# Kernel tuning notes

Measured on AMD Instinct MI355X. Metric: run time of the kernel, lower is better.

## Reference

```python
import jax, jax.numpy as jnp
import numpy as np

T = 256          # tokens
H = 1024         # hidden_size
E = 64           # num_experts
I = 512          # routed intermediate_size
SI = 2048        # shared_expert_intermediate_size
TOP_K = 6
N_GROUP = 8
TOPK_GROUP = 4
ROUTED_SCALE = 2.5


def setup_inputs() -> dict:
    key = jax.random.key(0)
    ks = jax.random.split(key, 9)
    s = 0.02
    return {
        "hidden_states": jax.random.normal(ks[0], (T, H), jnp.float32),
        "gate_w": jax.random.normal(ks[1], (E, H), jnp.float32) * s,
        "e_bias": jax.random.normal(ks[2], (E,), jnp.float32) * 0.01,
        "w1": jax.random.normal(ks[3], (E, I, H), jnp.float32) * s,  # gate proj
        "w3": jax.random.normal(ks[4], (E, I, H), jnp.float32) * s,  # up proj
        "w2": jax.random.normal(ks[5], (E, H, I), jnp.float32) * s,  # down proj
        "ws_gate": jax.random.normal(ks[6], (SI, H), jnp.float32) * s,
        "ws_up": jax.random.normal(ks[7], (SI, H), jnp.float32) * s,
        "ws_down": jax.random.normal(ks[8], (H, SI), jnp.float32) * s,
    }


def _noaux_tc_routing(logits, e_bias):
    # DeepSeek-V3 group-limited sigmoid routing (is_thop=False path).
    scores = jax.nn.sigmoid(logits)                         # [T, E]
    swb = scores + e_bias                                   # bias only picks experts
    t, e = scores.shape
    g = swb.reshape(t, N_GROUP, e // N_GROUP)
    group_scores = jax.lax.top_k(g, 2)[0].sum(-1)           # top-2 sum per group [T, G]
    _, gidx = jax.lax.top_k(group_scores, TOPK_GROUP)
    gmask = jax.nn.one_hot(gidx, N_GROUP, dtype=scores.dtype).sum(-2)  # [T, G]
    smask = jnp.repeat(gmask, e // N_GROUP, axis=-1)        # [T, E]
    _, tidx = jax.lax.top_k(swb * smask, TOP_K)
    nmask = jax.nn.one_hot(tidx, e, dtype=scores.dtype).sum(-2)
    s = scores * nmask
    s = s / (s.sum(-1, keepdims=True) + 1e-20) * ROUTED_SCALE  # [T, E], TOP_K nonzeros
    # torch code returns topk(values, indices) of s; s itself is the dense
    # combine-weight matrix with exactly those values scattered at the indices.
    return s


def reference(hidden_states, gate_w, e_bias, w1, w3, w2, ws_gate, ws_up, ws_down):
    x = hidden_states
    # gate: cublas_mm with fp32 output
    logits = (x @ gate_w.T).astype(jnp.float32)             # [T, E]
    cw = _noaux_tc_routing(logits, e_bias)                  # [T, E] combine weights

    # routed experts: gated MLP per expert, combined by routing weights
    h1 = jnp.einsum('th,eih->tei', x, w1)
    h3 = jnp.einsum('th,eih->tei', x, w3)
    act = jax.nn.silu(h1) * h3                              # [T, E, I]
    eo = jnp.einsum('tei,ehi->teh', act, w2)                # [T, E, H]
    routed = jnp.einsum('teh,te->th', eo, cw.astype(x.dtype))

    # shared experts: GatedMLP
    shared = (jax.nn.silu(x @ ws_gate.T) * (x @ ws_up.T)) @ ws_down.T

    return shared + routed
```

## Files before the change

### kernel.cpp

```cpp
#include <hip/hip_runtime.h>
#include <math.h>

#define T_TOK 256
#define H_DIM 1024
#define E_NUM 64
#define I_DIM 512
#define SI_DIM 2048

#define BN 64
#define BM 32
#define BK 64
#define LDB 72

typedef __attribute__((ext_vector_type(8))) short short8;
typedef __attribute__((ext_vector_type(8))) __bf16 bf16x8;
typedef __attribute__((ext_vector_type(4))) float floatx4;
typedef __attribute__((ext_vector_type(4))) unsigned short ushort4v;

static __device__ __forceinline__ unsigned short f2bf(float f) {
  unsigned u = __float_as_uint(f);
  u += 0x7FFFu + ((u >> 16) & 1u);
  return (unsigned short)(u >> 16);
}

static __device__ __forceinline__ ushort4v pack4(floatx4 v) {
  ushort4v b;
  b[0] = f2bf(v[0]); b[1] = f2bf(v[1]); b[2] = f2bf(v[2]); b[3] = f2bf(v[3]);
  return b;
}

static __device__ __forceinline__ floatx4 mfma16(bf16x8 a, bf16x8 b, floatx4 c) {
  return __builtin_amdgcn_mfma_f32_16x16x32_bf16(a, b, c, 0, 0, 0);
}

__global__ __launch_bounds__(256) void gate_route_kernel(
    const float* __restrict__ x, const float* __restrict__ gw,
    const float* __restrict__ ebias, unsigned short* __restrict__ xbf,
    int* __restrict__ cnt, int* __restrict__ tok_list,
    float* __restrict__ wt_list) {
  const int t = blockIdx.x;
  const int j = threadIdx.x;
  __shared__ float xs[H_DIM];
  __shared__ double pd[4 * 64];

  floatx4 v = ((const floatx4*)(x + (size_t)t * H_DIM))[j];
  xs[4 * j + 0] = v[0]; xs[4 * j + 1] = v[1];
  xs[4 * j + 2] = v[2]; xs[4 * j + 3] = v[3];
  ((ushort4v*)(xbf + (size_t)t * H_DIM))[j] = pack4(v);
  __syncthreads();

  const int e = j & 63, ch = j >> 6;
  const float* wr = gw + (size_t)e * H_DIM + ch * 256;
  const float* xc = xs + ch * 256;
  double acc = 0.0;
  for (int i = 0; i < 64; ++i) {
    floatx4 w = ((const floatx4*)wr)[i];
    acc += (double)xc[4 * i + 0] * (double)w[0]
         + (double)xc[4 * i + 1] * (double)w[1]
         + (double)xc[4 * i + 2] * (double)w[2]
         + (double)xc[4 * i + 3] * (double)w[3];
  }
  pd[ch * 64 + e] = acc;
  __syncthreads();

  if (j < 64) {
    const int lane = j;
    const double logit = pd[lane] + pd[64 + lane] + pd[128 + lane] + pd[192 + lane];
    const double score = 1.0 / (1.0 + exp(-logit));
    const double swb = score + (double)ebias[lane];

    double m1 = swb, m2 = -1.0e300;
    #pragma unroll
    for (int d = 1; d < 8; d <<= 1) {
      double o1 = __shfl_xor(m1, d);
      double o2 = __shfl_xor(m2, d);
      double hi = fmax(m1, o1), lo = fmin(m1, o1);
      m1 = hi;
      m2 = fmax(lo, fmax(m2, o2));
    }
    const double gscore = m1 + m2;

    double gs[8];
    #pragma unroll
    for (int g = 0; g < 8; ++g) gs[g] = __shfl(gscore, g << 3);
    unsigned gsel = 0;
    #pragma unroll
    for (int it = 0; it < 4; ++it) {
      int best = 0; double bv = -1.0e300;
      #pragma unroll
      for (int g = 0; g < 8; ++g) {
        bool taken = (gsel >> g) & 1u;
        if (!taken && gs[g] > bv) { bv = gs[g]; best = g; }
      }
      gsel |= 1u << best;
    }

    double key = ((gsel >> (lane >> 3)) & 1u) ? swb : -1.0e300;
    int selected = 0;
    for (int it = 0; it < 6; ++it) {
      double vv = key; int idx = lane;
      #pragma unroll
      for (int d = 1; d < 64; d <<= 1) {
        double ov = __shfl_xor(vv, d);
        int oi = __shfl_xor(idx, d);
        if (ov > vv || (ov == vv && oi < idx)) { vv = ov; idx = oi; }
      }
      if (lane == idx) { selected = 1; key = -1.0e300; }
    }

    double ssum = selected ? score : 0.0;
    #pragma unroll
    for (int d = 1; d < 64; d <<= 1) ssum += __shfl_xor(ssum, d);

    if (selected) {
      float wgt = (float)(score / (ssum + 1e-20) * 2.5);
      int p = atomicAdd(&cnt[lane], 1);
      tok_list[lane * T_TOK + p] = t;
      wt_list[lane * T_TOK + p] = wgt;
    }
  }
}

__global__ __launch_bounds__(256) void routed_gu_kernel(
    const unsigned short* __restrict__ xbf, const float* __restrict__ w1,
    const float* __restrict__ w3, const int* __restrict__ cnt,
    const int* __restrict__ tok_list, unsigned short* __restrict__ act_r) {
  __shared__ unsigned short sBg[BN * LDB];
  __shared__ unsigned short sBu[BN * LDB];
  __shared__ unsigned short sA[BM * LDB];
  __shared__ int stok[BM];

  const int e = blockIdx.x >> 3;
  const int n0 = (blockIdx.x & 7) * BN;
  const int j = threadIdx.x;
  const int wv = j >> 6, lane = j & 63;
  const int q = lane >> 4, c = lane & 15;
  const int ne = cnt[e];
  const int* tl = tok_list + e * T_TOK;
  unsigned short* ap = act_r + (size_t)e * T_TOK * I_DIM;
  const float* wgB = w1 + ((size_t)e * I_DIM + n0) * H_DIM;
  const float* wuB = w3 + ((size_t)e * I_DIM + n0) * H_DIM;

  const int wrow = j >> 4;
  const int wcol = (j & 15) * 4;
  const int arow = j >> 3;
  const int acol = (j & 7) * 8;

  for (int m0 = 0; m0 < ne; m0 += BM) {
    __syncthreads();
    if (j < BM) {
      int r = m0 + j;
      stok[j] = (r < ne) ? tl[r] : 0;
    }
    floatx4 ag0 = (floatx4)0.0f, ag1 = (floatx4)0.0f;
    floatx4 au0 = (floatx4)0.0f, au1 = (floatx4)0.0f;
    for (int k0 = 0; k0 < H_DIM; k0 += BK) {
      __syncthreads();
      #pragma unroll
      for (int p = 0; p < 4; ++p) {
        const int r = p * 16 + wrow;
        floatx4 g = *(const floatx4*)(wgB + (size_t)r * H_DIM + k0 + wcol);
        floatx4 u = *(const floatx4*)(wuB + (size_t)r * H_DIM + k0 + wcol);
        *(ushort4v*)(sBg + r * LDB + wcol) = pack4(g);
        *(ushort4v*)(sBu + r * LDB + wcol) = pack4(u);
      }
      *(bf16x8*)(sA + arow * LDB + acol) =
          *(const bf16x8*)(xbf + (size_t)stok[arow] * H_DIM + k0 + acol);
      __syncthreads();
      #pragma unroll
      for (int kk = 0; kk < BK; kk += 32) {
        const int ko = kk + q * 8;
        bf16x8 bg = *(const bf16x8*)(sBg + (wv * 16 + c) * LDB + ko);
        bf16x8 bu = *(const bf16x8*)(sBu + (wv * 16 + c) * LDB + ko);
        bf16x8 a0 = *(const bf16x8*)(sA + c * LDB + ko);
        bf16x8 a1 = *(const bf16x8*)(sA + (16 + c) * LDB + ko);
        ag0 = mfma16(a0, bg, ag0);
        ag1 = mfma16(a1, bg, ag1);
        au0 = mfma16(a0, bu, au0);
        au1 = mfma16(a1, bu, au1);
      }
    }
    #pragma unroll
    for (int s = 0; s < 2; ++s) {
      floatx4 g = s ? ag1 : ag0;
      floatx4 u = s ? au1 : au0;
      #pragma unroll
      for (int r = 0; r < 4; ++r) {
        const int m = m0 + s * 16 + q * 4 + r;
        if (m < ne) {
          float gg = g[r], uu = u[r];
          float a = gg / (1.0f + __expf(-gg)) * uu;
          ap[(size_t)m * I_DIM + n0 + wv * 16 + c] = f2bf(a);
        }
      }
    }
  }
}

__global__ __launch_bounds__(256) void shared_gu_kernel(
    const unsigned short* __restrict__ xbf, const float* __restrict__ wsg,
    const float* __restrict__ wsu, unsigned short* __restrict__ act_s) {
  __shared__ unsigned short sBg[BN * LDB];
  __shared__ unsigned short sBu[BN * LDB];
  __shared__ unsigned short sA[BM * LDB];

  const int n0 = (blockIdx.x & 31) * BN;
  const int m0 = (blockIdx.x >> 5) * BM;
  const int j = threadIdx.x;
  const int wv = j >> 6, lane = j & 63;
  const int q = lane >> 4, c = lane & 15;
  const float* wgB = wsg + (size_t)n0 * H_DIM;
  const float* wuB = wsu + (size_t)n0 * H_DIM;

  const int wrow = j >> 4, wcol = (j & 15) * 4;
  const int arow = j >> 3, acol = (j & 7) * 8;

  floatx4 ag0 = (floatx4)0.0f, ag1 = (floatx4)0.0f;
  floatx4 au0 = (floatx4)0.0f, au1 = (floatx4)0.0f;
  for (int k0 = 0; k0 < H_DIM; k0 += BK) {
    __syncthreads();
    #pragma unroll
    for (int p = 0; p < 4; ++p) {
      const int r = p * 16 + wrow;
      floatx4 g = *(const floatx4*)(wgB + (size_t)r * H_DIM + k0 + wcol);
      floatx4 u = *(const floatx4*)(wuB + (size_t)r * H_DIM + k0 + wcol);
      *(ushort4v*)(sBg + r * LDB + wcol) = pack4(g);
      *(ushort4v*)(sBu + r * LDB + wcol) = pack4(u);
    }
    *(bf16x8*)(sA + arow * LDB + acol) =
        *(const bf16x8*)(xbf + (size_t)(m0 + arow) * H_DIM + k0 + acol);
    __syncthreads();
    #pragma unroll
    for (int kk = 0; kk < BK; kk += 32) {
      const int ko = kk + q * 8;
      bf16x8 bg = *(const bf16x8*)(sBg + (wv * 16 + c) * LDB + ko);
      bf16x8 bu = *(const bf16x8*)(sBu + (wv * 16 + c) * LDB + ko);
      bf16x8 a0 = *(const bf16x8*)(sA + c * LDB + ko);
      bf16x8 a1 = *(const bf16x8*)(sA + (16 + c) * LDB + ko);
      ag0 = mfma16(a0, bg, ag0);
      ag1 = mfma16(a1, bg, ag1);
      au0 = mfma16(a0, bu, au0);
      au1 = mfma16(a1, bu, au1);
    }
  }
  #pragma unroll
  for (int s = 0; s < 2; ++s) {
    floatx4 g = s ? ag1 : ag0;
    floatx4 u = s ? au1 : au0;
    #pragma unroll
    for (int r = 0; r < 4; ++r) {
      const int m = m0 + s * 16 + q * 4 + r;
      float gg = g[r], uu = u[r];
      float a = gg / (1.0f + __expf(-gg)) * uu;
      act_s[(size_t)m * SI_DIM + n0 + wv * 16 + c] = f2bf(a);
    }
  }
}

__global__ __launch_bounds__(256) void shared_down_kernel(
    const unsigned short* __restrict__ act_s, const float* __restrict__ wsd,
    float* __restrict__ out) {
  __shared__ unsigned short sB[BN * LDB];
  __shared__ unsigned short sA[BM * LDB];

  const int n0 = (blockIdx.x & 15) * BN;
  const int m0 = ((blockIdx.x >> 4) & 7) * BM;
  const int kh = blockIdx.x >> 7;
  const int kbeg = kh * (SI_DIM / 2);
  const int j = threadIdx.x;
  const int wv = j >> 6, lane = j & 63;
  const int q = lane >> 4, c = lane & 15;
  const float* wB = wsd + (size_t)n0 * SI_DIM;

  const int wrow = j >> 4, wcol = (j & 15) * 4;
  const int arow = j >> 3, acol = (j & 7) * 8;

  floatx4 ac0 = (floatx4)0.0f, ac1 = (floatx4)0.0f;
  for (int k0 = kbeg; k0 < kbeg + SI_DIM / 2; k0 += BK) {
    __syncthreads();
    #pragma unroll
    for (int p = 0; p < 4; ++p) {
      const int r = p * 16 + wrow;
      floatx4 w = *(const floatx4*)(wB + (size_t)r * SI_DIM + k0 + wcol);
      *(ushort4v*)(sB + r * LDB + wcol) = pack4(w);
    }
    *(bf16x8*)(sA + arow * LDB + acol) =
        *(const bf16x8*)(act_s + (size_t)(m0 + arow) * SI_DIM + k0 + acol);
    __syncthreads();
    #pragma unroll
    for (int kk = 0; kk < BK; kk += 32) {
      const int ko = kk + q * 8;
      bf16x8 b = *(const bf16x8*)(sB + (wv * 16 + c) * LDB + ko);
      bf16x8 a0 = *(const bf16x8*)(sA + c * LDB + ko);
      bf16x8 a1 = *(const bf16x8*)(sA + (16 + c) * LDB + ko);
      ac0 = mfma16(a0, b, ac0);
      ac1 = mfma16(a1, b, ac1);
    }
  }
  #pragma unroll
  for (int s = 0; s < 2; ++s) {
    floatx4 d = s ? ac1 : ac0;
    #pragma unroll
    for (int r = 0; r < 4; ++r) {
      const int m = m0 + s * 16 + q * 4 + r;
      atomicAdd(&out[(size_t)m * H_DIM + n0 + wv * 16 + c], d[r]);
    }
  }
}

__global__ __launch_bounds__(256) void routed_down_kernel(
    const unsigned short* __restrict__ act_r, const float* __restrict__ w2,
    const int* __restrict__ cnt, const int* __restrict__ tok_list,
    const float* __restrict__ wt_list, float* __restrict__ out) {
  __shared__ unsigned short sB[BN * LDB];
  __shared__ unsigned short sA[BM * LDB];
  __shared__ int stok[BM];
  __shared__ float swl[BM];

  const int e = blockIdx.x >> 4;
  const int n0 = (blockIdx.x & 15) * BN;
  const int j = threadIdx.x;
  const int wv = j >> 6, lane = j & 63;
  const int q = lane >> 4, c = lane & 15;
  const int ne = cnt[e];
  const int* tl = tok_list + e * T_TOK;
  const float* wl = wt_list + e * T_TOK;
  const unsigned short* apb = act_r + (size_t)e * T_TOK * I_DIM;
  const float* wB = w2 + ((size_t)e * H_DIM + n0) * I_DIM;

  const int wrow = j >> 4, wcol = (j & 15) * 4;
  const int arow = j >> 3, acol = (j & 7) * 8;

  for (int m0 = 0; m0 < ne; m0 += BM) {
    __syncthreads();
    if (j < BM) {
      int r = m0 + j;
      bool ok = r < ne;
      stok[j] = ok ? tl[r] : 0;
      swl[j] = ok ? wl[r] : 0.0f;
    }
    floatx4 ac0 = (floatx4)0.0f, ac1 = (floatx4)0.0f;
    for (int k0 = 0; k0 < I_DIM; k0 += BK) {
      __syncthreads();
      #pragma unroll
      for (int p = 0; p < 4; ++p) {
        const int r = p * 16 + wrow;
        floatx4 w = *(const floatx4*)(wB + (size_t)r * I_DIM + k0 + wcol);
        *(ushort4v*)(sB + r * LDB + wcol) = pack4(w);
      }
      int ar = m0 + arow;
      if (ar >= T_TOK) ar = T_TOK - 1;
      *(bf16x8*)(sA + arow * LDB + acol) =
          *(const bf16x8*)(apb + (size_t)ar * I_DIM + k0 + acol);
      __syncthreads();
      #pragma unroll
      for (int kk = 0; kk < BK; kk += 32) {
        const int ko = kk + q * 8;
        bf16x8 b = *(const bf16x8*)(sB + (wv * 16 + c) * LDB + ko);
        bf16x8 a0 = *(const bf16x8*)(sA + c * LDB + ko);
        bf16x8 a1 = *(const bf16x8*)(sA + (16 + c) * LDB + ko);
        ac0 = mfma16(a0, b, ac0);
        ac1 = mfma16(a1, b, ac1);
      }
    }
    #pragma unroll
    for (int s = 0; s < 2; ++s) {
      floatx4 d = s ? ac1 : ac0;
      #pragma unroll
      for (int r = 0; r < 4; ++r) {
        const int mi = s * 16 + q * 4 + r;
        if (m0 + mi < ne) {
          atomicAdd(&out[(size_t)stok[mi] * H_DIM + n0 + wv * 16 + c],
                    d[r] * swl[mi]);
        }
      }
    }
  }
}

extern "C" void kernel_launch(void* const* d_in, const int* in_sizes, int n_in,
                              void* d_out, int out_size, void* d_ws, size_t ws_size,
                              hipStream_t stream) {
  const float* x   = (const float*)d_in[0];
  const float* gw  = (const float*)d_in[1];
  const float* eb  = (const float*)d_in[2];
  const float* w1  = (const float*)d_in[3];
  const float* w3  = (const float*)d_in[4];
  const float* w2  = (const float*)d_in[5];
  const float* wsg = (const float*)d_in[6];
  const float* wsu = (const float*)d_in[7];
  const float* wsd = (const float*)d_in[8];
  float* out = (float*)d_out;

  char* ws = (char*)d_ws;
  unsigned short* xbf   = (unsigned short*)(ws);
  unsigned short* act_s = (unsigned short*)(ws + 524288);
  int*   cnt            = (int*)(ws + 1572864);
  int*   tok            = (int*)(ws + 1573120);
  float* wt             = (float*)(ws + 1638656);
  unsigned short* act_r = (unsigned short*)(ws + 1704192);

  hipMemsetAsync(cnt, 0, E_NUM * sizeof(int), stream);
  hipMemsetAsync(out, 0, (size_t)T_TOK * H_DIM * sizeof(float), stream);
  gate_route_kernel<<<dim3(T_TOK), dim3(256), 0, stream>>>(x, gw, eb, xbf, cnt, tok, wt);
  routed_gu_kernel<<<dim3(E_NUM * (I_DIM / BN)), dim3(256), 0, stream>>>(xbf, w1, w3, cnt, tok, act_r);
  shared_gu_kernel<<<dim3((SI_DIM / BN) * (T_TOK / BM)), dim3(256), 0, stream>>>(xbf, wsg, wsu, act_s);
  shared_down_kernel<<<dim3((H_DIM / BN) * (T_TOK / BM) * 2), dim3(256), 0, stream>>>(act_s, wsd, out);
  routed_down_kernel<<<dim3(E_NUM * (H_DIM / BN)), dim3(256), 0, stream>>>(act_r, w2, cnt, tok, wt, out);
}
```

Measured before the change: 555.3 us.

## Register-prefetch next K tile in all four GEMM kernels

Each GEMM kernel now loads the next K-slice of fp32 weights and bf16 activations into registers while the MFMA loop consumes the current shared-memory tile, then packs and stores them at the top of the next iteration. This hides global load latency behind compute in these weight-bandwidth-bound kernels. Launch bounds also add a minimum of 2 blocks per CU, which caps registers at a time when the prefetch buffers raise register pressure and could cause spills.

Result: faster. 466.2 us (-16.0%).

```diff
diff --git a/kernel.cpp b/kernel.cpp
--- a/kernel.cpp
+++ b/kernel.cpp
@@ -121,7 +121,7 @@
   }
 }
 
-__global__ __launch_bounds__(256) void routed_gu_kernel(
+__global__ __launch_bounds__(256, 2) void routed_gu_kernel(
     const unsigned short* __restrict__ xbf, const float* __restrict__ w1,
     const float* __restrict__ w3, const int* __restrict__ cnt,
     const int* __restrict__ tok_list, unsigned short* __restrict__ act_r) {
@@ -152,21 +152,38 @@
       int r = m0 + j;
       stok[j] = (r < ne) ? tl[r] : 0;
     }
+    __syncthreads();
+    const unsigned short* aRow = xbf + (size_t)stok[arow] * H_DIM;
+
+    floatx4 pg[4], pu[4];
+    bf16x8 pa;
+    #pragma unroll
+    for (int p = 0; p < 4; ++p) {
+      pg[p] = *(const floatx4*)(wgB + (size_t)(p * 16 + wrow) * H_DIM + wcol);
+      pu[p] = *(const floatx4*)(wuB + (size_t)(p * 16 + wrow) * H_DIM + wcol);
+    }
+    pa = *(const bf16x8*)(aRow + acol);
+
     floatx4 ag0 = (floatx4)0.0f, ag1 = (floatx4)0.0f;
     floatx4 au0 = (floatx4)0.0f, au1 = (floatx4)0.0f;
     for (int k0 = 0; k0 < H_DIM; k0 += BK) {
+      if (k0) __syncthreads();
+      #pragma unroll
+      for (int p = 0; p < 4; ++p) {
+        *(ushort4v*)(sBg + (p * 16 + wrow) * LDB + wcol) = pack4(pg[p]);
+        *(ushort4v*)(sBu + (p * 16 + wrow) * LDB + wcol) = pack4(pu[p]);
+      }
+      *(bf16x8*)(sA + arow * LDB + acol) = pa;
       __syncthreads();
-      #pragma unroll
-      for (int p = 0; p < 4; ++p) {
-        const int r = p * 16 + wrow;
-        floatx4 g = *(const floatx4*)(wgB + (size_t)r * H_DIM + k0 + wcol);
-        floatx4 u = *(const floatx4*)(wuB + (size_t)r * H_DIM + k0 + wcol);
-        *(ushort4v*)(sBg + r * LDB + wcol) = pack4(g);
-        *(ushort4v*)(sBu + r * LDB + wcol) = pack4(u);
-      }
-      *(bf16x8*)(sA + arow * LDB + acol) =
-          *(const bf16x8*)(xbf + (size_t)stok[arow] * H_DIM + k0 + acol);
-      __syncthreads();
+      if (k0 + BK < H_DIM) {
+        const int kn = k0 + BK;
+        #pragma unroll
+        for (int p = 0; p < 4; ++p) {
+          pg[p] = *(const floatx4*)(wgB + (size_t)(p * 16 + wrow) * H_DIM + kn + wcol);
+          pu[p] = *(const floatx4*)(wuB + (size_t)(p * 16 + wrow) * H_DIM + kn + wcol);
+        }
+        pa = *(const bf16x8*)(aRow + kn + acol);
+      }
       #pragma unroll
       for (int kk = 0; kk < BK; kk += 32) {
         const int ko = kk + q * 8;
@@ -197,7 +214,7 @@
   }
 }
 
-__global__ __launch_bounds__(256) void shared_gu_kernel(
+__global__ __launch_bounds__(256, 2) void shared_gu_kernel(
     const unsigned short* __restrict__ xbf, const float* __restrict__ wsg,
     const float* __restrict__ wsu, unsigned short* __restrict__ act_s) {
   __shared__ unsigned short sBg[BN * LDB];
@@ -214,22 +231,37 @@
 
   const int wrow = j >> 4, wcol = (j & 15) * 4;
   const int arow = j >> 3, acol = (j & 7) * 8;
+  const unsigned short* aRow = xbf + (size_t)(m0 + arow) * H_DIM;
+
+  floatx4 pg[4], pu[4];
+  bf16x8 pa;
+  #pragma unroll
+  for (int p = 0; p < 4; ++p) {
+    pg[p] = *(const floatx4*)(wgB + (size_t)(p * 16 + wrow) * H_DIM + wcol);
+    pu[p] = *(const floatx4*)(wuB + (size_t)(p * 16 + wrow) * H_DIM + wcol);
+  }
+  pa = *(const bf16x8*)(aRow + acol);
 
   floatx4 ag0 = (floatx4)0.0f, ag1 = (floatx4)0.0f;
   floatx4 au0 = (floatx4)0.0f, au1 = (floatx4)0.0f;
   for (int k0 = 0; k0 < H_DIM; k0 += BK) {
+    if (k0) __syncthreads();
+    #pragma unroll
+    for (int p = 0; p < 4; ++p) {
+      *(ushort4v*)(sBg + (p * 16 + wrow) * LDB + wcol) = pack4(pg[p]);
+      *(ushort4v*)(sBu + (p * 16 + wrow) * LDB + wcol) = pack4(pu[p]);
+    }
+    *(bf16x8*)(sA + arow * LDB + acol) = pa;
     __syncthreads();
-    #pragma unroll
-    for (int p = 0; p < 4; ++p) {
-      const int r = p * 16 + wrow;
-      floatx4 g = *(const floatx4*)(wgB + (size_t)r * H_DIM + k0 + wcol);
-      floatx4 u = *(const floatx4*)(wuB + (size_t)r * H_DIM + k0 + wcol);
-      *(ushort4v*)(sBg + r * LDB + wcol) = pack4(g);
-      *(ushort4v*)(sBu + r * LDB + wcol) = pack4(u);
-    }
-    *(bf16x8*)(sA + arow * LDB + acol) =
-        *(const bf16x8*)(xbf + (size_t)(m0 + arow) * H_DIM + k0 + acol);
-    __syncthreads();
+    if (k0 + BK < H_DIM) {
+      const int kn = k0 + BK;
+      #pragma unroll
+      for (int p = 0; p < 4; ++p) {
+        pg[p] = *(const floatx4*)(wgB + (size_t)(p * 16 + wrow) * H_DIM + kn + wcol);
+        pu[p] = *(const floatx4*)(wuB + (size_t)(p * 16 + wrow) * H_DIM + kn + wcol);
+      }
+      pa = *(const bf16x8*)(aRow + kn + acol);
+    }
     #pragma unroll
     for (int kk = 0; kk < BK; kk += 32) {
       const int ko = kk + q * 8;
@@ -257,7 +289,7 @@
   }
 }
 
-__global__ __launch_bounds__(256) void shared_down_kernel(
+__global__ __launch_bounds__(256, 2) void shared_down_kernel(
     const unsigned short* __restrict__ act_s, const float* __restrict__ wsd,
     float* __restrict__ out) {
   __shared__ unsigned short sB[BN * LDB];
@@ -274,19 +306,34 @@
 
   const int wrow = j >> 4, wcol = (j & 15) * 4;
   const int arow = j >> 3, acol = (j & 7) * 8;
+  const unsigned short* aRow = act_s + (size_t)(m0 + arow) * SI_DIM;
+
+  floatx4 pw[4];
+  bf16x8 pa;
+  #pragma unroll
+  for (int p = 0; p < 4; ++p) {
+    pw[p] = *(const floatx4*)(wB + (size_t)(p * 16 + wrow) * SI_DIM + kbeg + wcol);
+  }
+  pa = *(const bf16x8*)(aRow + kbeg + acol);
 
   floatx4 ac0 = (floatx4)0.0f, ac1 = (floatx4)0.0f;
-  for (int k0 = kbeg; k0 < kbeg + SI_DIM / 2; k0 += BK) {
+  for (int kr = 0; kr < SI_DIM / 2; kr += BK) {
+    const int k0 = kbeg + kr;
+    if (kr) __syncthreads();
+    #pragma unroll
+    for (int p = 0; p < 4; ++p) {
+      *(ushort4v*)(sB + (p * 16 + wrow) * LDB + wcol) = pack4(pw[p]);
+    }
+    *(bf16x8*)(sA + arow * LDB + acol) = pa;
     __syncthreads();
-    #pragma unroll
-    for (int p = 0; p < 4; ++p) {
-      const int r = p * 16 + wrow;
-      floatx4 w = *(const floatx4*)(wB + (size_t)r * SI_DIM + k0 + wcol);
-      *(ushort4v*)(sB + r * LDB + wcol) = pack4(w);
-    }
-    *(bf16x8*)(sA + arow * LDB + acol) =
-        *(const bf16x8*)(act_s + (size_t)(m0 + arow) * SI_DIM + k0 + acol);
-    __syncthreads();
+    if (kr + BK < SI_DIM / 2) {
+      const int kn = k0 + BK;
+      #pragma unroll
+      for (int p = 0; p < 4; ++p) {
+        pw[p] = *(const floatx4*)(wB + (size_t)(p * 16 + wrow) * SI_DIM + kn + wcol);
+      }
+      pa = *(const bf16x8*)(aRow + kn + acol);
+    }
     #pragma unroll
     for (int kk = 0; kk < BK; kk += 32) {
       const int ko = kk + q * 8;
@@ -308,7 +355,7 @@
   }
 }
 
-__global__ __launch_bounds__(256) void routed_down_kernel(
+__global__ __launch_bounds__(256, 2) void routed_down_kernel(
     const unsigned short* __restrict__ act_r, const float* __restrict__ w2,
     const int* __restrict__ cnt, const int* __restrict__ tok_list,
     const float* __restrict__ wt_list, float* __restrict__ out) {
@@ -339,20 +386,35 @@
       stok[j] = ok ? tl[r] : 0;
       swl[j] = ok ? wl[r] : 0.0f;
     }
+    int ar = m0 + arow;
+    if (ar >= T_TOK) ar = T_TOK - 1;
+    const unsigned short* aRow = apb + (size_t)ar * I_DIM;
+
+    floatx4 pw[4];
+    bf16x8 pa;
+    #pragma unroll
+    for (int p = 0; p < 4; ++p) {
+      pw[p] = *(const floatx4*)(wB + (size_t)(p * 16 + wrow) * I_DIM + wcol);
+    }
+    pa = *(const bf16x8*)(aRow + acol);
+
     floatx4 ac0 = (floatx4)0.0f, ac1 = (floatx4)0.0f;
     for (int k0 = 0; k0 < I_DIM; k0 += BK) {
       __syncthreads();
       #pragma unroll
       for (int p = 0; p < 4; ++p) {
-        const int r = p * 16 + wrow;
-        floatx4 w = *(const floatx4*)(wB + (size_t)r * I_DIM + k0 + wcol);
-        *(ushort4v*)(sB + r * LDB + wcol) = pack4(w);
-      }
-      int ar = m0 + arow;
-      if (ar >= T_TOK) ar = T_TOK - 1;
-      *(bf16x8*)(sA + arow * LDB + acol) =
-          *(const bf16x8*)(apb + (size_t)ar * I_DIM + k0 + acol);
+        *(ushort4v*)(sB + (p * 16 + wrow) * LDB + wcol) = pack4(pw[p]);
+      }
+      *(bf16x8*)(sA + arow * LDB + acol) = pa;
       __syncthreads();
+      if (k0 + BK < I_DIM) {
+        const int kn = k0 + BK;
+        #pragma unroll
+        for (int p = 0; p < 4; ++p) {
+          pw[p] = *(const floatx4*)(wB + (size_t)(p * 16 + wrow) * I_DIM + kn + wcol);
+        }
+        pa = *(const bf16x8*)(aRow + kn + acol);
+      }
       #pragma unroll
       for (int kk = 0; kk < BK; kk += 32) {
         const int ko = kk + q * 8;
```
